# Optimization experiments

Measured on AMD Instinct MI355X. Metric: run time of the kernel, lower is better.

The kernel has to match this reference:

```python
import jax, jax.numpy as jnp
import numpy as np
import math

BATCH, SEQ, D_CONTENT = 16, 512, 1024
D_POSITION, NUM_TILES, D_HIDDEN = 64, 8, 4096


def _make_pe(max_len, d_model):
    pe = np.zeros((max_len, d_model), dtype=np.float32)
    position = np.arange(max_len, dtype=np.float32)[:, None]
    div_term = np.exp(np.arange(0, d_model, 2, dtype=np.float32) * (-math.log(10000.0) / d_model))
    pe[:, 0::2] = np.sin(position * div_term)
    pe[:, 1::2] = np.cos(position * div_term)
    return jnp.asarray(pe)


def setup_inputs() -> dict:
    key = jax.random.key(0)
    ks = jax.random.split(key, 8)
    x = jax.random.normal(ks[0], (BATCH, SEQ, D_CONTENT), dtype=jnp.float32)
    pe = _make_pe(SEQ, D_POSITION)  # (SEQ, D_POSITION), buffer sliced to seq len
    position_weight = jnp.asarray(0.5, dtype=jnp.float32)
    content_weight = jnp.asarray(0.5, dtype=jnp.float32)
    pos_sigs = jax.random.normal(ks[1], (NUM_TILES, D_POSITION), dtype=jnp.float32)
    content_sigs = jax.random.normal(ks[2], (NUM_TILES, D_CONTENT), dtype=jnp.float32)
    s1 = 1.0 / math.sqrt(D_CONTENT)
    s2 = 1.0 / math.sqrt(D_HIDDEN)
    W1 = jax.random.normal(ks[3], (NUM_TILES, D_CONTENT, D_HIDDEN), dtype=jnp.float32) * s1
    b1 = jax.random.normal(ks[4], (NUM_TILES, D_HIDDEN), dtype=jnp.float32) * s1
    W2 = jax.random.normal(ks[5], (NUM_TILES, D_HIDDEN, D_CONTENT), dtype=jnp.float32) * s2
    b2 = jax.random.normal(ks[6], (NUM_TILES, D_CONTENT), dtype=jnp.float32) * s2
    return {"x": x, "pe": pe, "position_weight": position_weight,
            "content_weight": content_weight, "pos_sigs": pos_sigs,
            "content_sigs": content_sigs, "W1": W1, "b1": b1, "W2": W2, "b2": b2}


def reference(x, pe, position_weight, content_weight, pos_sigs, content_sigs, W1, b1, W2, b2):
    B, S, _ = x.shape
    num_tiles = W1.shape[0]
    # normalized position/content mixing weights
    pw = jax.nn.sigmoid(position_weight)
    cw = jax.nn.sigmoid(content_weight)
    tot = pw + cw
    pw, cw = pw / tot, cw / tot
    # mixed address: [pw * pos_enc | cw * x] -> (B, S, Dp + Dc)
    pos_part = jnp.broadcast_to((pw * pe[:S])[None], (B, S, pe.shape[-1]))
    address = jnp.concatenate([pos_part, cw * x], axis=-1)
    # ternarized signatures (T, Dp + Dc)
    signatures = jnp.concatenate([jnp.sign(pos_sigs), jnp.sign(content_sigs)], axis=-1)
    scores = jnp.einsum('bsd,td->bst', address, signatures)
    indices = jnp.argmax(scores, axis=-1)  # (B, S) top-1 tile per token
    # dispatch: per-tile gelu MLP, combined via top-1 mask (loop over fixed small tile count)
    out = jnp.zeros_like(x)
    for t in range(num_tiles):
        h = jax.nn.gelu(jnp.einsum('bsd,dh->bsh', x, W1[t]) + b1[t], approximate=False)
        y = jnp.einsum('bsh,hd->bsd', h, W2[t]) + b2[t]
        out = out + jnp.where((indices == t)[..., None], y, jnp.zeros((), x.dtype))
    return out
```

## Files before the change

### kernel.cpp

```cpp
#include <hip/hip_runtime.h>
#include <hip/hip_bf16.h>
#include <math.h>

#define BATCH 16
#define SEQ   512
#define DC    1024
#define DP    64
#define NT    8
#define DH    4096
#define NTOK  (BATCH*SEQ)

#define BM 128
#define BN 128
#define BK 32

typedef __attribute__((ext_vector_type(8))) short short8;
typedef __attribute__((ext_vector_type(4))) float floatx4;
typedef __attribute__((ext_vector_type(4))) unsigned short ushort4v;
typedef __attribute__((ext_vector_type(8))) unsigned short ushort8v;

__device__ __forceinline__ unsigned short f2bf(float f) {
  union { float f; unsigned u; } v; v.f = f;
  unsigned r = v.u + 0x7FFFu + ((v.u >> 16) & 1u);
  return (unsigned short)(r >> 16);
}

__device__ __forceinline__ void gl_lds16(const void* g, void* l) {
  __builtin_amdgcn_global_load_lds(
      (__attribute__((address_space(1))) void*)g,
      (__attribute__((address_space(3))) void*)l, 16, 0, 0);
}

__global__ __launch_bounds__(256) void route_kernel(
    const float* __restrict__ x, const float* __restrict__ pe,
    const float* __restrict__ pwp, const float* __restrict__ cwp,
    const float* __restrict__ pos_sigs, const float* __restrict__ csigs,
    int* __restrict__ counts, int* __restrict__ list,
    unsigned short* __restrict__ xb) {
  int wid  = threadIdx.x >> 6;
  int lane = threadIdx.x & 63;
  int token = blockIdx.x * 4 + wid;
  int s = token & (SEQ - 1);

  float pwr = 1.f / (1.f + expf(-pwp[0]));
  float cwr = 1.f / (1.f + expf(-cwp[0]));
  float tot = pwr + cwr;
  float pw = pwr / tot, cw = cwr / tot;

  float acc[NT];
#pragma unroll
  for (int t = 0; t < NT; t++) acc[t] = 0.f;

  float a0 = pw * pe[s * DP + lane];
#pragma unroll
  for (int t = 0; t < NT; t++) {
    float v = pos_sigs[t * DP + lane];
    float sg = (v > 0.f) ? 1.f : ((v < 0.f) ? -1.f : 0.f);
    acc[t] = fmaf(a0, sg, acc[t]);
  }

  const float* xrow = x + (size_t)token * DC;
  unsigned short* xbrow = xb + (size_t)token * DC;
#pragma unroll 4
  for (int i = 0; i < DC / 64; i++) {
    int c = lane + i * 64;
    float xv = xrow[c];
    xbrow[c] = f2bf(xv);
    float a = cw * xv;
#pragma unroll
    for (int t = 0; t < NT; t++) {
      float v = csigs[t * DC + c];
      float sg = (v > 0.f) ? 1.f : ((v < 0.f) ? -1.f : 0.f);
      acc[t] = fmaf(a, sg, acc[t]);
    }
  }

#pragma unroll
  for (int off = 32; off >= 1; off >>= 1)
#pragma unroll
    for (int t = 0; t < NT; t++) acc[t] += __shfl_xor(acc[t], off);

  if (lane == 0) {
    int best = 0; float bv = acc[0];
#pragma unroll
    for (int t = 1; t < NT; t++)
      if (acc[t] > bv) { bv = acc[t]; best = t; }
    int slot = atomicAdd(&counts[best], 1);
    list[best * NTOK + slot] = token;
  }
}

template<int AR, int AC>
__global__ __launch_bounds__(256) void transpose_kernel(
    const float* __restrict__ in, unsigned short* __restrict__ out) {
  __shared__ unsigned short tile[64 * 65];
  int t = blockIdx.z;
  const float* in_t = in + (size_t)t * AR * AC;
  unsigned short* out_t = out + (size_t)t * AR * AC;
  int x0 = blockIdx.x * 64, y0 = blockIdx.y * 64;
  int tid = threadIdx.x;
  int ry = tid >> 2, cx = (tid & 3) * 16;
  const float* src = in_t + (size_t)(y0 + ry) * AC + x0 + cx;
  float4 v0 = *(const float4*)(src);
  float4 v1 = *(const float4*)(src + 4);
  float4 v2 = *(const float4*)(src + 8);
  float4 v3 = *(const float4*)(src + 12);
  unsigned short* trow = &tile[ry * 65 + cx];
  trow[0]  = f2bf(v0.x); trow[1]  = f2bf(v0.y); trow[2]  = f2bf(v0.z); trow[3]  = f2bf(v0.w);
  trow[4]  = f2bf(v1.x); trow[5]  = f2bf(v1.y); trow[6]  = f2bf(v1.z); trow[7]  = f2bf(v1.w);
  trow[8]  = f2bf(v2.x); trow[9]  = f2bf(v2.y); trow[10] = f2bf(v2.z); trow[11] = f2bf(v2.w);
  trow[12] = f2bf(v3.x); trow[13] = f2bf(v3.y); trow[14] = f2bf(v3.z); trow[15] = f2bf(v3.w);
  __syncthreads();
  int rx = tid >> 2, cy = (tid & 3) * 16;
  ushort8v o0, o1;
#pragma unroll
  for (int j = 0; j < 8; j++) o0[j] = tile[(cy + j) * 65 + rx];
#pragma unroll
  for (int j = 0; j < 8; j++) o1[j] = tile[(cy + 8 + j) * 65 + rx];
  size_t ob = (size_t)(x0 + rx) * AR + y0 + cy;
  *(ushort8v*)&out_t[ob]     = o0;
  *(ushort8v*)&out_t[ob + 8] = o1;
}

template<int K, int N, bool GELU>
__global__ __launch_bounds__(256) void gemm_async_kernel(
    const unsigned short* __restrict__ A, const unsigned short* __restrict__ BT,
    const float* __restrict__ bias, const int* __restrict__ counts,
    const int* __restrict__ list, unsigned short* __restrict__ Hout,
    float* __restrict__ Fout) {
  int t = blockIdx.z;
  int count = counts[t];
  int base = blockIdx.y * BM;
  if (base >= count) return;
  int j0 = blockIdx.x * BN;

  __shared__ unsigned short As[BM * BK];
  __shared__ unsigned short Bs[BN * BK];
  __shared__ int toks[BM];

  int tid = threadIdx.x;
  if (tid < BM) {
    int slot = base + tid;
    toks[tid] = (slot < count) ? list[t * NTOK + slot] : -1;
  }
  __syncthreads();

  int w = tid >> 6, lane = tid & 63;
  int lrow = lane >> 2;
  int lc   = lane & 3;
  int swz  = (lc ^ (lrow & 3)) * 8;

  const unsigned short* srcA[2];
  const unsigned short* srcB[2];
  unsigned short* dstA[2];
  unsigned short* dstB[2];
#pragma unroll
  for (int i = 0; i < 2; i++) {
    int ch = i * 4 + w;
    int r = ch * 16 + lrow;
    int tk = toks[r]; if (tk < 0) tk = 0;
    srcA[i] = A + (size_t)tk * K + swz;
    srcB[i] = BT + (size_t)t * N * K + (size_t)(j0 + r) * K + swz;
    dstA[i] = &As[ch * 512];
    dstB[i] = &Bs[ch * 512];
  }

  int wm = (w & 1) * 64, wn = (w >> 1) * 64;
  int quad = lane >> 4, l15 = lane & 15;
  int fswz = (quad ^ (l15 & 3)) * 8;

  floatx4 acc[4][4];
#pragma unroll
  for (int mi = 0; mi < 4; mi++)
#pragma unroll
    for (int ni = 0; ni < 4; ni++) acc[mi][ni] = (floatx4){0.f, 0.f, 0.f, 0.f};

  for (int k0 = 0; k0 < K; k0 += BK) {
#pragma unroll
    for (int i = 0; i < 2; i++) {
      gl_lds16(srcA[i], dstA[i]);
      gl_lds16(srcB[i], dstB[i]);
      srcA[i] += BK; srcB[i] += BK;
    }
    __syncthreads();

    short8 a[4], b[4];
#pragma unroll
    for (int mi = 0; mi < 4; mi++)
      a[mi] = *(const short8*)&As[(wm + mi * 16 + l15) * BK + fswz];
#pragma unroll
    for (int ni = 0; ni < 4; ni++)
      b[ni] = *(const short8*)&Bs[(wn + ni * 16 + l15) * BK + fswz];
#pragma unroll
    for (int mi = 0; mi < 4; mi++)
#pragma unroll
      for (int ni = 0; ni < 4; ni++)
        acc[mi][ni] = __builtin_amdgcn_mfma_f32_16x16x32_bf16(a[mi], b[ni], acc[mi][ni], 0, 0, 0);
    __syncthreads();
  }

#pragma unroll
  for (int ni = 0; ni < 4; ni++) {
    int n = j0 + wn + ni * 16 + l15;
    float bv = bias[t * N + n];
#pragma unroll
    for (int mi = 0; mi < 4; mi++) {
      int mb = wm + mi * 16 + quad * 4;
#pragma unroll
      for (int r = 0; r < 4; r++) {
        int tok = toks[mb + r];
        if (tok >= 0) {
          float v = acc[mi][ni][r] + bv;
          if (GELU) {
            v = 0.5f * v * (1.f + erff(v * 0.70710678118654752f));
            Hout[(size_t)tok * N + n] = f2bf(v);
          } else {
            Fout[(size_t)tok * N + n] = v;
          }
        }
      }
    }
  }
}

#define KPAD 40
__global__ __launch_bounds__(256) void gemm1_fb(
    const unsigned short* __restrict__ xb, const float* __restrict__ W1,
    const float* __restrict__ b1, const int* __restrict__ counts,
    const int* __restrict__ list, unsigned short* __restrict__ H) {
  int t = blockIdx.z;
  int count = counts[t];
  int base = blockIdx.y * BM;
  if (base >= count) return;
  int j0 = blockIdx.x * BN;
  __shared__ unsigned short As[BM][KPAD];
  __shared__ unsigned short Bs[BN][KPAD];
  __shared__ int toks[BM];
  int tid = threadIdx.x;
  if (tid < BM) {
    int slot = base + tid;
    toks[tid] = (slot < count) ? list[t * NTOK + slot] : -1;
  }
  __syncthreads();
  int arow = tid >> 1, acol = (tid & 1) * 16;
  int mytok = toks[arow];
  const unsigned short* xrow = xb + (size_t)(mytok < 0 ? 0 : mytok) * DC;
  int kg4 = (tid >> 5) * 4, ng4 = (tid & 31) * 4;
  const float* Wt = W1 + (size_t)t * DC * DH;
  int wid = tid >> 6, lane = tid & 63;
  int wm = (wid & 1) * 64, wn = (wid >> 1) * 64;
  int quad = lane >> 4, l15 = lane & 15;
  floatx4 acc[4][4];
#pragma unroll
  for (int mi = 0; mi < 4; mi++)
#pragma unroll
    for (int ni = 0; ni < 4; ni++) acc[mi][ni] = (floatx4){0.f, 0.f, 0.f, 0.f};
  for (int kt = 0; kt < DC / BK; kt++) {
    int k0 = kt * BK;
    if (mytok >= 0) {
      *(uint4*)&As[arow][acol]     = *(const uint4*)(xrow + k0 + acol);
      *(uint4*)&As[arow][acol + 8] = *(const uint4*)(xrow + k0 + acol + 8);
    } else {
      uint4 z = {0u,0u,0u,0u};
      *(uint4*)&As[arow][acol] = z; *(uint4*)&As[arow][acol + 8] = z;
    }
    const float* wb = Wt + (size_t)(k0 + kg4) * DH + j0 + ng4;
    float4 r0 = *(const float4*)(wb);
    float4 r1 = *(const float4*)(wb + DH);
    float4 r2 = *(const float4*)(wb + 2 * DH);
    float4 r3 = *(const float4*)(wb + 3 * DH);
    ushort4v c0 = { f2bf(r0.x), f2bf(r1.x), f2bf(r2.x), f2bf(r3.x) };
    ushort4v c1 = { f2bf(r0.y), f2bf(r1.y), f2bf(r2.y), f2bf(r3.y) };
    ushort4v c2 = { f2bf(r0.z), f2bf(r1.z), f2bf(r2.z), f2bf(r3.z) };
    ushort4v c3 = { f2bf(r0.w), f2bf(r1.w), f2bf(r2.w), f2bf(r3.w) };
    *(ushort4v*)&Bs[ng4 + 0][kg4] = c0; *(ushort4v*)&Bs[ng4 + 1][kg4] = c1;
    *(ushort4v*)&Bs[ng4 + 2][kg4] = c2; *(ushort4v*)&Bs[ng4 + 3][kg4] = c3;
    __syncthreads();
    short8 a[4], b[4];
#pragma unroll
    for (int mi = 0; mi < 4; mi++) a[mi] = *(const short8*)&As[wm + mi * 16 + l15][quad * 8];
#pragma unroll
    for (int ni = 0; ni < 4; ni++) b[ni] = *(const short8*)&Bs[wn + ni * 16 + l15][quad * 8];
#pragma unroll
    for (int mi = 0; mi < 4; mi++)
#pragma unroll
      for (int ni = 0; ni < 4; ni++)
        acc[mi][ni] = __builtin_amdgcn_mfma_f32_16x16x32_bf16(a[mi], b[ni], acc[mi][ni], 0, 0, 0);
    __syncthreads();
  }
#pragma unroll
  for (int ni = 0; ni < 4; ni++) {
    int n = j0 + wn + ni * 16 + l15;
    float bias = b1[t * DH + n];
#pragma unroll
    for (int mi = 0; mi < 4; mi++) {
      int mb = wm + mi * 16 + quad * 4;
#pragma unroll
      for (int r = 0; r < 4; r++) {
        int tok = toks[mb + r];
        if (tok >= 0) {
          float v = acc[mi][ni][r] + bias;
          v = 0.5f * v * (1.f + erff(v * 0.70710678118654752f));
          H[(size_t)tok * DH + n] = f2bf(v);
        }
      }
    }
  }
}

__global__ __launch_bounds__(256) void gemm2_fb(
    const unsigned short* __restrict__ H, const float* __restrict__ W2,
    const float* __restrict__ b2, const int* __restrict__ counts,
    const int* __restrict__ list, float* __restrict__ out) {
  int t = blockIdx.z;
  int count = counts[t];
  int base = blockIdx.y * BM;
  if (base >= count) return;
  int j0 = blockIdx.x * BN;
  __shared__ unsigned short As[BM][KPAD];
  __shared__ unsigned short Bs[BN][KPAD];
  __shared__ int toks[BM];
  int tid = threadIdx.x;
  if (tid < BM) {
    int slot = base + tid;
    toks[tid] = (slot < count) ? list[t * NTOK + slot] : -1;
  }
  __syncthreads();
  int arow = tid >> 1, acol = (tid & 1) * 16;
  int mytok = toks[arow];
  const unsigned short* hrow = H + (size_t)(mytok < 0 ? 0 : mytok) * DH;
  int kg4 = (tid >> 5) * 4, ng4 = (tid & 31) * 4;
  const float* Wt = W2 + (size_t)t * DH * DC;
  int wid = tid >> 6, lane = tid & 63;
  int wm = (wid & 1) * 64, wn = (wid >> 1) * 64;
  int quad = lane >> 4, l15 = lane & 15;
  floatx4 acc[4][4];
#pragma unroll
  for (int mi = 0; mi < 4; mi++)
#pragma unroll
    for (int ni = 0; ni < 4; ni++) acc[mi][ni] = (floatx4){0.f, 0.f, 0.f, 0.f};
  for (int kt = 0; kt < DH / BK; kt++) {
    int k0 = kt * BK;
    if (mytok >= 0) {
      *(uint4*)&As[arow][acol]     = *(const uint4*)(hrow + k0 + acol);
      *(uint4*)&As[arow][acol + 8] = *(const uint4*)(hrow + k0 + acol + 8);
    } else {
      uint4 z = {0u,0u,0u,0u};
      *(uint4*)&As[arow][acol] = z; *(uint4*)&As[arow][acol + 8] = z;
    }
    const float* wb = Wt + (size_t)(k0 + kg4) * DC + j0 + ng4;
    float4 r0 = *(const float4*)(wb);
    float4 r1 = *(const float4*)(wb + DC);
    float4 r2 = *(const float4*)(wb + 2 * DC);
    float4 r3 = *(const float4*)(wb + 3 * DC);
    ushort4v c0 = { f2bf(r0.x), f2bf(r1.x), f2bf(r2.x), f2bf(r3.x) };
    ushort4v c1 = { f2bf(r0.y), f2bf(r1.y), f2bf(r2.y), f2bf(r3.y) };
    ushort4v c2 = { f2bf(r0.z), f2bf(r1.z), f2bf(r2.z), f2bf(r3.z) };
    ushort4v c3 = { f2bf(r0.w), f2bf(r1.w), f2bf(r2.w), f2bf(r3.w) };
    *(ushort4v*)&Bs[ng4 + 0][kg4] = c0; *(ushort4v*)&Bs[ng4 + 1][kg4] = c1;
    *(ushort4v*)&Bs[ng4 + 2][kg4] = c2; *(ushort4v*)&Bs[ng4 + 3][kg4] = c3;
    __syncthreads();
    short8 a[4], b[4];
#pragma unroll
    for (int mi = 0; mi < 4; mi++) a[mi] = *(const short8*)&As[wm + mi * 16 + l15][quad * 8];
#pragma unroll
    for (int ni = 0; ni < 4; ni++) b[ni] = *(const short8*)&Bs[wn + ni * 16 + l15][quad * 8];
#pragma unroll
    for (int mi = 0; mi < 4; mi++)
#pragma unroll
      for (int ni = 0; ni < 4; ni++)
        acc[mi][ni] = __builtin_amdgcn_mfma_f32_16x16x32_bf16(a[mi], b[ni], acc[mi][ni], 0, 0, 0);
    __syncthreads();
  }
#pragma unroll
  for (int ni = 0; ni < 4; ni++) {
    int n = j0 + wn + ni * 16 + l15;
    float bias = b2[t * DC + n];
#pragma unroll
    for (int mi = 0; mi < 4; mi++) {
      int mb = wm + mi * 16 + quad * 4;
#pragma unroll
      for (int r = 0; r < 4; r++) {
        int tok = toks[mb + r];
        if (tok >= 0) out[(size_t)tok * DC + n] = acc[mi][ni][r] + bias;
      }
    }
  }
}

extern "C" void kernel_launch(void* const* d_in, const int* in_sizes, int n_in,
                              void* d_out, int out_size, void* d_ws, size_t ws_size,
                              hipStream_t stream) {
  const float* x        = (const float*)d_in[0];
  const float* pe       = (const float*)d_in[1];
  const float* pwp      = (const float*)d_in[2];
  const float* cwp      = (const float*)d_in[3];
  const float* pos_sigs = (const float*)d_in[4];
  const float* csigs    = (const float*)d_in[5];
  const float* W1       = (const float*)d_in[6];
  const float* b1       = (const float*)d_in[7];
  const float* W2       = (const float*)d_in[8];
  const float* b2       = (const float*)d_in[9];
  float* out = (float*)d_out;

  char* ws = (char*)d_ws;
  int* counts = (int*)ws;
  int* list   = (int*)(ws + 1024);
  unsigned short* xb = (unsigned short*)(ws + (1 << 20));

  hipMemsetAsync(counts, 0, NT * sizeof(int), stream);
  route_kernel<<<NTOK / 4, 256, 0, stream>>>(x, pe, pwp, cwp, pos_sigs, csigs,
                                             counts, list, xb);

  if (ws_size >= (size_t)145 * 1024 * 1024) {
    unsigned short* WT = (unsigned short*)(ws + ((size_t)17 << 20));
    unsigned short* H  = (unsigned short*)(ws + ((size_t)81 << 20));

    transpose_kernel<DC, DH><<<dim3(DH / 64, DC / 64, NT), 256, 0, stream>>>(W1, WT);
    gemm_async_kernel<DC, DH, true><<<dim3(DH / BN, NTOK / BM, NT), 256, 0, stream>>>(
        xb, WT, b1, counts, list, H, nullptr);
    transpose_kernel<DH, DC><<<dim3(DC / 64, DH / 64, NT), 256, 0, stream>>>(W2, WT);
    gemm_async_kernel<DH, DC, false><<<dim3(DC / BN, NTOK / BM, NT), 256, 0, stream>>>(
        H, WT, b2, counts, list, nullptr, out);
  } else {
    unsigned short* H = (unsigned short*)(ws + ((size_t)32 << 20));
    gemm1_fb<<<dim3(DH / BN, NTOK / BM, NT), 256, 0, stream>>>(xb, W1, b1, counts, list, H);
    gemm2_fb<<<dim3(DC / BN, NTOK / BM, NT), 256, 0, stream>>>(H, W2, b2, counts, list, out);
  }
}
```

Measured before the change: 706.7 us.

## Double-buffer LDS in grouped GEMM to overlap async loads with MFMA

Splits the A and B shared-memory tiles into two buffers so the global-to-LDS async copy for the next K-step is issued while MFMAs run on the current one. This halves the barriers per K-step and hides load latency. It also changes the swizzle pattern to cut LDS bank conflicts, raises wave priority around the MFMA block, and adds an occupancy hint to launch bounds. Doubled LDS use may lower occupancy.

```diff
diff --git a/kernel.cpp b/kernel.cpp
--- a/kernel.cpp
+++ b/kernel.cpp
@@ -122,8 +122,39 @@
   *(ushort8v*)&out_t[ob + 8] = o1;
 }
 
+
+__device__ __forceinline__ void stage_step(
+    const unsigned short* (&srcA)[2], const unsigned short* (&srcB)[2],
+    unsigned short* dA, unsigned short* dB, const int (&cho)[2]) {
+#pragma unroll
+  for (int i = 0; i < 2; i++) {
+    gl_lds16(srcA[i], dA + cho[i]);
+    gl_lds16(srcB[i], dB + cho[i]);
+    srcA[i] += BK; srcB[i] += BK;
+  }
+}
+
+__device__ __forceinline__ void mfma_tile(
+    const unsigned short* __restrict__ Ab, const unsigned short* __restrict__ Bb,
+    int wm, int wn, int l15, int fswz, floatx4 (&acc)[4][4]) {
+  short8 a[4], b[4];
+#pragma unroll
+  for (int mi = 0; mi < 4; mi++)
+    a[mi] = *(const short8*)&Ab[(wm + mi * 16 + l15) * BK + fswz];
+#pragma unroll
+  for (int ni = 0; ni < 4; ni++)
+    b[ni] = *(const short8*)&Bb[(wn + ni * 16 + l15) * BK + fswz];
+  __builtin_amdgcn_s_setprio(1);
+#pragma unroll
+  for (int mi = 0; mi < 4; mi++)
+#pragma unroll
+    for (int ni = 0; ni < 4; ni++)
+      acc[mi][ni] = __builtin_amdgcn_mfma_f32_16x16x32_bf16(a[mi], b[ni], acc[mi][ni], 0, 0, 0);
+  __builtin_amdgcn_s_setprio(0);
+}
+
 template<int K, int N, bool GELU>
-__global__ __launch_bounds__(256) void gemm_async_kernel(
+__global__ __launch_bounds__(256, 4) void gemm_async_kernel(
     const unsigned short* __restrict__ A, const unsigned short* __restrict__ BT,
     const float* __restrict__ bias, const int* __restrict__ counts,
     const int* __restrict__ list, unsigned short* __restrict__ Hout,
@@ -134,8 +165,8 @@
   if (base >= count) return;
   int j0 = blockIdx.x * BN;
 
-  __shared__ unsigned short As[BM * BK];
-  __shared__ unsigned short Bs[BN * BK];
+  __shared__ __align__(16) unsigned short As[2][BM * BK];
+  __shared__ __align__(16) unsigned short Bs[2][BN * BK];
   __shared__ int toks[BM];
 
   int tid = threadIdx.x;
@@ -148,12 +179,11 @@
   int w = tid >> 6, lane = tid & 63;
   int lrow = lane >> 2;
   int lc   = lane & 3;
-  int swz  = (lc ^ (lrow & 3)) * 8;
+  int swz  = (lc ^ ((lrow >> 1) & 3)) * 8;
 
   const unsigned short* srcA[2];
   const unsigned short* srcB[2];
-  unsigned short* dstA[2];
-  unsigned short* dstB[2];
+  int cho[2];
 #pragma unroll
   for (int i = 0; i < 2; i++) {
     int ch = i * 4 + w;
@@ -161,13 +191,12 @@
     int tk = toks[r]; if (tk < 0) tk = 0;
     srcA[i] = A + (size_t)tk * K + swz;
     srcB[i] = BT + (size_t)t * N * K + (size_t)(j0 + r) * K + swz;
-    dstA[i] = &As[ch * 512];
-    dstB[i] = &Bs[ch * 512];
+    cho[i] = ch * 512;
   }
 
   int wm = (w & 1) * 64, wn = (w >> 1) * 64;
   int quad = lane >> 4, l15 = lane & 15;
-  int fswz = (quad ^ (l15 & 3)) * 8;
+  int fswz = (quad ^ ((l15 >> 1) & 3)) * 8;
 
   floatx4 acc[4][4];
 #pragma unroll
@@ -175,29 +204,24 @@
 #pragma unroll
     for (int ni = 0; ni < 4; ni++) acc[mi][ni] = (floatx4){0.f, 0.f, 0.f, 0.f};
 
-  for (int k0 = 0; k0 < K; k0 += BK) {
-#pragma unroll
-    for (int i = 0; i < 2; i++) {
-      gl_lds16(srcA[i], dstA[i]);
-      gl_lds16(srcB[i], dstB[i]);
-      srcA[i] += BK; srcB[i] += BK;
-    }
-    __syncthreads();
-
-    short8 a[4], b[4];
-#pragma unroll
-    for (int mi = 0; mi < 4; mi++)
-      a[mi] = *(const short8*)&As[(wm + mi * 16 + l15) * BK + fswz];
-#pragma unroll
-    for (int ni = 0; ni < 4; ni++)
-      b[ni] = *(const short8*)&Bs[(wn + ni * 16 + l15) * BK + fswz];
-#pragma unroll
-    for (int mi = 0; mi < 4; mi++)
-#pragma unroll
-      for (int ni = 0; ni < 4; ni++)
-        acc[mi][ni] = __builtin_amdgcn_mfma_f32_16x16x32_bf16(a[mi], b[ni], acc[mi][ni], 0, 0, 0);
-    __syncthreads();
-  }
+  constexpr int S = K / BK;
+
+  stage_step(srcA, srcB, As[0], Bs[0], cho);
+  __syncthreads();
+
+  stage_step(srcA, srcB, As[1], Bs[1], cho);
+  mfma_tile(As[0], Bs[0], wm, wn, l15, fswz, acc);
+  __syncthreads();
+
+  for (int p = 0; p < (S - 2) / 2; p++) {
+    stage_step(srcA, srcB, As[0], Bs[0], cho);
+    mfma_tile(As[1], Bs[1], wm, wn, l15, fswz, acc);
+    __syncthreads();
+    stage_step(srcA, srcB, As[1], Bs[1], cho);
+    mfma_tile(As[0], Bs[0], wm, wn, l15, fswz, acc);
+    __syncthreads();
+  }
+  mfma_tile(As[1], Bs[1], wm, wn, l15, fswz, acc);
 
 #pragma unroll
   for (int ni = 0; ni < 4; ni++) {
```

Result: slower. 744.9 us (+5.4%).

## Add triple-buffered pipelined GEMM for first MLP layer and change LDS swizzle

Applied to the files above, without the earlier changes.

Adds a new GEMM kernel that keeps three LDS buffers for A and B tiles and issues the global-to-LDS loads for stage k+2 while MFMAs run on stage k. It uses explicit vmcnt waits and a single barrier per iteration, and raises wave priority around the MFMA block. The first GEMM (x·W1 with GELU) switches to this kernel, which is meant to hide memory latency and cut barrier stalls. The LDS swizzle also changes to XOR on (row>>1), aimed at reducing bank conflicts for 16-byte reads. The cost is three times the LDS per block, which may lower occupancy, and the hand-written waitcnt logic is fragile.

```diff
diff --git a/kernel.cpp b/kernel.cpp
--- a/kernel.cpp
+++ b/kernel.cpp
@@ -148,7 +148,7 @@
   int w = tid >> 6, lane = tid & 63;
   int lrow = lane >> 2;
   int lc   = lane & 3;
-  int swz  = (lc ^ (lrow & 3)) * 8;
+  int swz  = (lc ^ ((lrow >> 1) & 3)) * 8;
 
   const unsigned short* srcA[2];
   const unsigned short* srcB[2];
@@ -167,7 +167,7 @@
 
   int wm = (w & 1) * 64, wn = (w >> 1) * 64;
   int quad = lane >> 4, l15 = lane & 15;
-  int fswz = (quad ^ (l15 & 3)) * 8;
+  int fswz = (quad ^ ((l15 >> 1) & 3)) * 8;
 
   floatx4 acc[4][4];
 #pragma unroll
@@ -197,6 +197,151 @@
       for (int ni = 0; ni < 4; ni++)
         acc[mi][ni] = __builtin_amdgcn_mfma_f32_16x16x32_bf16(a[mi], b[ni], acc[mi][ni], 0, 0, 0);
     __syncthreads();
+  }
+
+#pragma unroll
+  for (int ni = 0; ni < 4; ni++) {
+    int n = j0 + wn + ni * 16 + l15;
+    float bv = bias[t * N + n];
+#pragma unroll
+    for (int mi = 0; mi < 4; mi++) {
+      int mb = wm + mi * 16 + quad * 4;
+#pragma unroll
+      for (int r = 0; r < 4; r++) {
+        int tok = toks[mb + r];
+        if (tok >= 0) {
+          float v = acc[mi][ni][r] + bv;
+          if (GELU) {
+            v = 0.5f * v * (1.f + erff(v * 0.70710678118654752f));
+            Hout[(size_t)tok * N + n] = f2bf(v);
+          } else {
+            Fout[(size_t)tok * N + n] = v;
+          }
+        }
+      }
+    }
+  }
+}
+
+template<int K, int N, bool GELU>
+__global__ __launch_bounds__(256) void gemm_pipe_kernel(
+    const unsigned short* __restrict__ A, const unsigned short* __restrict__ BT,
+    const float* __restrict__ bias, const int* __restrict__ counts,
+    const int* __restrict__ list, unsigned short* __restrict__ Hout,
+    float* __restrict__ Fout) {
+  int t = blockIdx.z;
+  int count = counts[t];
+  int base = blockIdx.y * BM;
+  if (base >= count) return;
+  int j0 = blockIdx.x * BN;
+
+  __shared__ __align__(16) unsigned short As[3][BM * BK];
+  __shared__ __align__(16) unsigned short Bs[3][BN * BK];
+  __shared__ int toks[BM];
+
+  int tid = threadIdx.x;
+  if (tid < BM) {
+    int slot = base + tid;
+    toks[tid] = (slot < count) ? list[t * NTOK + slot] : -1;
+  }
+  __syncthreads();
+
+  int w = tid >> 6, lane = tid & 63;
+  int lrow = lane >> 2;
+  int lc   = lane & 3;
+  int swz  = (lc ^ ((lrow >> 1) & 3)) * 8;
+
+  const unsigned short* srcA[2];
+  const unsigned short* srcB[2];
+  int cho[2];
+#pragma unroll
+  for (int i = 0; i < 2; i++) {
+    int ch = i * 4 + w;
+    int r = ch * 16 + lrow;
+    int tk = toks[r]; if (tk < 0) tk = 0;
+    srcA[i] = A + (size_t)tk * K + swz;
+    srcB[i] = BT + (size_t)t * N * K + (size_t)(j0 + r) * K + swz;
+    cho[i] = ch * 512;
+  }
+
+  int wm = (w & 1) * 64, wn = (w >> 1) * 64;
+  int quad = lane >> 4, l15 = lane & 15;
+  int fswz = (quad ^ ((l15 >> 1) & 3)) * 8;
+
+  floatx4 acc[4][4];
+#pragma unroll
+  for (int mi = 0; mi < 4; mi++)
+#pragma unroll
+    for (int ni = 0; ni < 4; ni++) acc[mi][ni] = (floatx4){0.f, 0.f, 0.f, 0.f};
+
+  constexpr int S = K / BK;
+  unsigned short *a0 = As[0], *a1 = As[1], *a2 = As[2];
+  unsigned short *b0 = Bs[0], *b1 = Bs[1], *b2 = Bs[2];
+
+#pragma unroll
+  for (int i = 0; i < 2; i++) {
+    gl_lds16(srcA[i], a0 + cho[i]); gl_lds16(srcB[i], b0 + cho[i]);
+    srcA[i] += BK; srcB[i] += BK;
+  }
+#pragma unroll
+  for (int i = 0; i < 2; i++) {
+    gl_lds16(srcA[i], a1 + cho[i]); gl_lds16(srcB[i], b1 + cho[i]);
+    srcA[i] += BK; srcB[i] += BK;
+  }
+  asm volatile("s_waitcnt vmcnt(4)" ::: "memory");
+  __builtin_amdgcn_s_barrier();
+
+#pragma unroll 1
+  for (int k = 0; k < S - 1; ++k) {
+    short8 a[4], b[4];
+#pragma unroll
+    for (int mi = 0; mi < 4; mi++)
+      a[mi] = *(const short8*)&a0[(wm + mi * 16 + l15) * BK + fswz];
+#pragma unroll
+    for (int ni = 0; ni < 4; ni++)
+      b[ni] = *(const short8*)&b0[(wn + ni * 16 + l15) * BK + fswz];
+
+    if (k < S - 2) {
+#pragma unroll
+      for (int i = 0; i < 2; i++) {
+        gl_lds16(srcA[i], a2 + cho[i]); gl_lds16(srcB[i], b2 + cho[i]);
+        srcA[i] += BK; srcB[i] += BK;
+      }
+    }
+
+    __builtin_amdgcn_s_setprio(1);
+#pragma unroll
+    for (int mi = 0; mi < 4; mi++)
+#pragma unroll
+      for (int ni = 0; ni < 4; ni++)
+        acc[mi][ni] = __builtin_amdgcn_mfma_f32_16x16x32_bf16(a[mi], b[ni], acc[mi][ni], 0, 0, 0);
+    __builtin_amdgcn_s_setprio(0);
+
+    if (k < S - 2) {
+      asm volatile("s_waitcnt vmcnt(4)" ::: "memory");
+    } else {
+      asm volatile("s_waitcnt vmcnt(0)" ::: "memory");
+    }
+    __builtin_amdgcn_s_barrier();
+
+    unsigned short* tp;
+    tp = a0; a0 = a1; a1 = a2; a2 = tp;
+    tp = b0; b0 = b1; b1 = b2; b2 = tp;
+  }
+
+  {
+    short8 a[4], b[4];
+#pragma unroll
+    for (int mi = 0; mi < 4; mi++)
+      a[mi] = *(const short8*)&a0[(wm + mi * 16 + l15) * BK + fswz];
+#pragma unroll
+    for (int ni = 0; ni < 4; ni++)
+      b[ni] = *(const short8*)&b0[(wn + ni * 16 + l15) * BK + fswz];
+#pragma unroll
+    for (int mi = 0; mi < 4; mi++)
+#pragma unroll
+      for (int ni = 0; ni < 4; ni++)
+        acc[mi][ni] = __builtin_amdgcn_mfma_f32_16x16x32_bf16(a[mi], b[ni], acc[mi][ni], 0, 0, 0);
   }
 
 #pragma unroll
@@ -417,7 +562,7 @@
     unsigned short* H  = (unsigned short*)(ws + ((size_t)81 << 20));
 
     transpose_kernel<DC, DH><<<dim3(DH / 64, DC / 64, NT), 256, 0, stream>>>(W1, WT);
-    gemm_async_kernel<DC, DH, true><<<dim3(DH / BN, NTOK / BM, NT), 256, 0, stream>>>(
+    gemm_pipe_kernel<DC, DH, true><<<dim3(DH / BN, NTOK / BM, NT), 256, 0, stream>>>(
         xb, WT, b1, counts, list, H, nullptr);
     transpose_kernel<DH, DC><<<dim3(DC / 64, DH / 64, NT), 256, 0, stream>>>(W2, WT);
     gemm_async_kernel<DH, DC, false><<<dim3(DC / BN, NTOK / BM, NT), 256, 0, stream>>>(
```

Result: no change. 699.0 us (-1.1%).

## Triple-buffer LDS in routed MoE GEMMs and interleave tiles across blocks

Applied to the files above, without the earlier changes.

Replaces the single-buffered load/compute loop with a three-stage LDS ring. Global-to-LDS async loads for stage k+2 are issued while MFMAs run on stage k, and fine-grained vmcnt waits take the place of two full barriers per iteration. The grid is flattened with the tile index in the low bits so blocks from different experts interleave, and the LDS swizzle pattern is changed to cut bank conflicts. The cost is three times the LDS per block, which may lower occupancy.

```diff
diff --git a/kernel.cpp b/kernel.cpp
--- a/kernel.cpp
+++ b/kernel.cpp
@@ -122,20 +122,25 @@
   *(ushort8v*)&out_t[ob + 8] = o1;
 }
 
-template<int K, int N, bool GELU>
-__global__ __launch_bounds__(256) void gemm_async_kernel(
+template<int K, int N, int NXB, bool GELU>
+__global__ __launch_bounds__(256) void gemm_pipe_kernel(
     const unsigned short* __restrict__ A, const unsigned short* __restrict__ BT,
     const float* __restrict__ bias, const int* __restrict__ counts,
     const int* __restrict__ list, unsigned short* __restrict__ Hout,
     float* __restrict__ Fout) {
-  int t = blockIdx.z;
+  unsigned bid = blockIdx.x;
+  int t = bid & (NT - 1);
+  unsigned inner = bid >> 3;
+  int bx = inner & (NXB - 1);
+  int by = inner / NXB;
+
   int count = counts[t];
-  int base = blockIdx.y * BM;
+  int base = by * BM;
   if (base >= count) return;
-  int j0 = blockIdx.x * BN;
-
-  __shared__ unsigned short As[BM * BK];
-  __shared__ unsigned short Bs[BN * BK];
+  int j0 = bx * BN;
+
+  __shared__ __align__(16) unsigned short As[3][BM * BK];
+  __shared__ __align__(16) unsigned short Bs[3][BN * BK];
   __shared__ int toks[BM];
 
   int tid = threadIdx.x;
@@ -148,12 +153,11 @@
   int w = tid >> 6, lane = tid & 63;
   int lrow = lane >> 2;
   int lc   = lane & 3;
-  int swz  = (lc ^ (lrow & 3)) * 8;
+  int swz  = (lc ^ ((lrow >> 1) & 3)) * 8;
 
   const unsigned short* srcA[2];
   const unsigned short* srcB[2];
-  unsigned short* dstA[2];
-  unsigned short* dstB[2];
+  int cho[2];
 #pragma unroll
   for (int i = 0; i < 2; i++) {
     int ch = i * 4 + w;
@@ -161,13 +165,12 @@
     int tk = toks[r]; if (tk < 0) tk = 0;
     srcA[i] = A + (size_t)tk * K + swz;
     srcB[i] = BT + (size_t)t * N * K + (size_t)(j0 + r) * K + swz;
-    dstA[i] = &As[ch * 512];
-    dstB[i] = &Bs[ch * 512];
+    cho[i] = ch * 512;
   }
 
   int wm = (w & 1) * 64, wn = (w >> 1) * 64;
   int quad = lane >> 4, l15 = lane & 15;
-  int fswz = (quad ^ (l15 & 3)) * 8;
+  int fswz = (quad ^ ((l15 >> 1) & 3)) * 8;
 
   floatx4 acc[4][4];
 #pragma unroll
@@ -175,28 +178,74 @@
 #pragma unroll
     for (int ni = 0; ni < 4; ni++) acc[mi][ni] = (floatx4){0.f, 0.f, 0.f, 0.f};
 
-  for (int k0 = 0; k0 < K; k0 += BK) {
-#pragma unroll
-    for (int i = 0; i < 2; i++) {
-      gl_lds16(srcA[i], dstA[i]);
-      gl_lds16(srcB[i], dstB[i]);
-      srcA[i] += BK; srcB[i] += BK;
-    }
-    __syncthreads();
-
+  constexpr int S = K / BK;
+  unsigned short *a0 = As[0], *a1 = As[1], *a2 = As[2];
+  unsigned short *b0 = Bs[0], *b1 = Bs[1], *b2 = Bs[2];
+
+#pragma unroll
+  for (int i = 0; i < 2; i++) {
+    gl_lds16(srcA[i], a0 + cho[i]); gl_lds16(srcB[i], b0 + cho[i]);
+    srcA[i] += BK; srcB[i] += BK;
+  }
+#pragma unroll
+  for (int i = 0; i < 2; i++) {
+    gl_lds16(srcA[i], a1 + cho[i]); gl_lds16(srcB[i], b1 + cho[i]);
+    srcA[i] += BK; srcB[i] += BK;
+  }
+  asm volatile("s_waitcnt vmcnt(4)" ::: "memory");
+  __builtin_amdgcn_s_barrier();
+
+#pragma unroll 1
+  for (int k = 0; k < S - 1; ++k) {
     short8 a[4], b[4];
 #pragma unroll
     for (int mi = 0; mi < 4; mi++)
-      a[mi] = *(const short8*)&As[(wm + mi * 16 + l15) * BK + fswz];
+      a[mi] = *(const short8*)&a0[(wm + mi * 16 + l15) * BK + fswz];
 #pragma unroll
     for (int ni = 0; ni < 4; ni++)
-      b[ni] = *(const short8*)&Bs[(wn + ni * 16 + l15) * BK + fswz];
+      b[ni] = *(const short8*)&b0[(wn + ni * 16 + l15) * BK + fswz];
+
+    if (k < S - 2) {
+#pragma unroll
+      for (int i = 0; i < 2; i++) {
+        gl_lds16(srcA[i], a2 + cho[i]); gl_lds16(srcB[i], b2 + cho[i]);
+        srcA[i] += BK; srcB[i] += BK;
+      }
+    }
+
+    __builtin_amdgcn_s_setprio(1);
 #pragma unroll
     for (int mi = 0; mi < 4; mi++)
 #pragma unroll
       for (int ni = 0; ni < 4; ni++)
         acc[mi][ni] = __builtin_amdgcn_mfma_f32_16x16x32_bf16(a[mi], b[ni], acc[mi][ni], 0, 0, 0);
-    __syncthreads();
+    __builtin_amdgcn_s_setprio(0);
+
+    if (k < S - 2) {
+      asm volatile("s_waitcnt vmcnt(4)" ::: "memory");
+    } else {
+      asm volatile("s_waitcnt vmcnt(0)" ::: "memory");
+    }
+    __builtin_amdgcn_s_barrier();
+
+    unsigned short* tp;
+    tp = a0; a0 = a1; a1 = a2; a2 = tp;
+    tp = b0; b0 = b1; b1 = b2; b2 = tp;
+  }
+
+  {
+    short8 a[4], b[4];
+#pragma unroll
+    for (int mi = 0; mi < 4; mi++)
+      a[mi] = *(const short8*)&a0[(wm + mi * 16 + l15) * BK + fswz];
+#pragma unroll
+    for (int ni = 0; ni < 4; ni++)
+      b[ni] = *(const short8*)&b0[(wn + ni * 16 + l15) * BK + fswz];
+#pragma unroll
+    for (int mi = 0; mi < 4; mi++)
+#pragma unroll
+      for (int ni = 0; ni < 4; ni++)
+        acc[mi][ni] = __builtin_amdgcn_mfma_f32_16x16x32_bf16(a[mi], b[ni], acc[mi][ni], 0, 0, 0);
   }
 
 #pragma unroll
@@ -417,10 +466,12 @@
     unsigned short* H  = (unsigned short*)(ws + ((size_t)81 << 20));
 
     transpose_kernel<DC, DH><<<dim3(DH / 64, DC / 64, NT), 256, 0, stream>>>(W1, WT);
-    gemm_async_kernel<DC, DH, true><<<dim3(DH / BN, NTOK / BM, NT), 256, 0, stream>>>(
+    gemm_pipe_kernel<DC, DH, DH / BN, true>
+        <<<(DH / BN) * (NTOK / BM) * NT, 256, 0, stream>>>(
         xb, WT, b1, counts, list, H, nullptr);
     transpose_kernel<DH, DC><<<dim3(DC / 64, DH / 64, NT), 256, 0, stream>>>(W2, WT);
-    gemm_async_kernel<DH, DC, false><<<dim3(DC / BN, NTOK / BM, NT), 256, 0, stream>>>(
+    gemm_pipe_kernel<DH, DC, DC / BN, false>
+        <<<(DC / BN) * (NTOK / BM) * NT, 256, 0, stream>>>(
         H, WT, b2, counts, list, nullptr, out);
   } else {
     unsigned short* H = (unsigned short*)(ws + ((size_t)32 << 20));
```

Result: no change. 698.7 us (-1.1%).
